# Kernel tuning notes

Measured on AMD Instinct MI355X. Metric: run time of the kernel, lower is better.

## Reference

```python
import jax, jax.numpy as jnp
import numpy as np

N_EMBD = 2048
N_HEAD = 16
HEAD_DIM = N_EMBD // N_HEAD
BATCH = 2
SEQ = 2048


def setup_inputs() -> dict:
    key = jax.random.key(0)
    k1, k2, k3 = jax.random.split(key, 3)
    scale = 0.02
    return {
        "hidden_states": jax.random.normal(k1, (BATCH, SEQ, N_EMBD), dtype=jnp.float32),
        "c_attn_w": jax.random.normal(k2, (N_EMBD, 3 * N_EMBD), dtype=jnp.float32) * scale,
        "c_attn_b": jnp.zeros((3 * N_EMBD,), dtype=jnp.float32),
        "c_proj_w": jax.random.normal(k3, (N_EMBD, N_EMBD), dtype=jnp.float32) * scale,
        "c_proj_b": jnp.zeros((N_EMBD,), dtype=jnp.float32),
    }


def reference(hidden_states, c_attn_w, c_attn_b, c_proj_w, c_proj_b):
    B, S, E = hidden_states.shape
    # Fused QKV projection (Conv1D: x @ W + b)
    qkv = hidden_states @ c_attn_w + c_attn_b  # [B, S, 3E]
    q, k, v = jnp.split(qkv, 3, axis=-1)
    # split heads -> [B, H, S, D]
    def split_heads(t):
        return t.reshape(B, S, N_HEAD, HEAD_DIM).transpose(0, 2, 1, 3)
    q, k, v = split_heads(q), split_heads(k), split_heads(v)
    # scaled scores, causal mask, softmax (dropout p=0 -> identity)
    scores = jnp.einsum("bhqd,bhkd->bhqk", q, k) / jnp.asarray(
        HEAD_DIM ** 0.5, dtype=q.dtype)
    causal = jnp.tril(jnp.ones((S, S), dtype=bool))  # [S, S]
    mask_value = jnp.finfo(scores.dtype).min
    scores = jnp.where(causal[None, None, :, :], scores, mask_value)
    attn = jax.nn.softmax(scores, axis=-1)
    out = jnp.einsum("bhqk,bhkd->bhqd", attn, v)  # [B, H, S, D]
    # merge heads -> [B, S, E]
    out = out.transpose(0, 2, 1, 3).reshape(B, S, E)
    # output projection
    return out @ c_proj_w + c_proj_b
```

## Files before the change

### kernel.cpp

```cpp
#include <hip/hip_runtime.h>
#include <hip/hip_bf16.h>

typedef __bf16 bf16x8 __attribute__((ext_vector_type(8)));
typedef float f32x4 __attribute__((ext_vector_type(4)));

__device__ __forceinline__ float bf2f(unsigned short u) {
  union { unsigned int i; float f; } v; v.i = ((unsigned int)u) << 16; return v.f;
}
__device__ __forceinline__ unsigned short f2bf(float f) {
  union { unsigned int i; float f; } v; v.f = f;
  unsigned int i = v.i;
  return (unsigned short)((i + 0x7FFFu + ((i >> 16) & 1u)) >> 16);
}

typedef const __attribute__((address_space(1))) unsigned int* gas_ptr;
typedef __attribute__((address_space(3))) unsigned int* las_ptr;
__device__ __forceinline__ void gload_lds16(const unsigned short* g, unsigned short* l) {
  __builtin_amdgcn_global_load_lds((gas_ptr)(const void*)g, (las_ptr)(void*)l, 16, 0, 0);
}

__global__ __launch_bounds__(256) void prologue_k(const void* __restrict__ hidden,
                                                  const void* __restrict__ w_qkv,
                                                  const void* __restrict__ w_proj,
                                                  unsigned short* __restrict__ hidden_bf,
                                                  unsigned short* __restrict__ Wt_qkv,
                                                  unsigned short* __restrict__ Wt_proj,
                                                  int* __restrict__ flag) {
  __shared__ unsigned short tile[32][33];
  __shared__ int s4[4];
  const int t = threadIdx.x;
  {
    const unsigned short* h = (const unsigned short*)hidden;
    int cnt = 0;
    for (int i = t; i < 2048; i += 256) {
      unsigned short u = h[2 * i];
      int e = (u >> 7) & 0xFF;
      cnt += ((e >= 96 && e <= 140) || u == 0) ? 1 : 0;
    }
#pragma unroll
    for (int off = 1; off < 64; off <<= 1) cnt += __shfl_xor(cnt, off, 64);
    if ((t & 63) == 0) s4[t >> 6] = cnt;
  }
  __syncthreads();
  const int f = (s4[0] + s4[1] + s4[2] + s4[3]) >= 1800;
  if (blockIdx.x == 0 && t == 0) *flag = f;

  int bid = blockIdx.x;
  if (bid < 2048) {
    if (f) return;
    const float* src = (const float*)hidden;
    int base = bid * 4096;
#pragma unroll
    for (int k = 0; k < 16; k++) hidden_bf[base + t + 256 * k] = f2bf(src[base + t + 256 * k]);
    return;
  }
  const void* src; unsigned short* dst; int C, cx, cy;
  if (bid < 14336) { bid -= 2048;  src = w_qkv;  dst = Wt_qkv;  C = 6144; cx = bid % 192; cy = bid / 192; }
  else             { bid -= 14336; src = w_proj; dst = Wt_proj; C = 2048; cx = bid % 64;  cy = bid / 64;  }
  const int x = t & 31, y = t >> 5;
  const int r0 = cy * 32, c0 = cx * 32;
#pragma unroll
  for (int i = 0; i < 4; i++) {
    size_t idx = (size_t)(r0 + y + 8 * i) * C + c0 + x;
    tile[y + 8 * i][x] = f ? ((const unsigned short*)src)[idx]
                           : f2bf(((const float*)src)[idx]);
  }
  __syncthreads();
#pragma unroll
  for (int i = 0; i < 4; i++)
    dst[(size_t)(c0 + y + 8 * i) * 2048 + r0 + x] = tile[x][y + 8 * i];
}

__global__ __launch_bounds__(256) void gemm_bias_k(const unsigned short* __restrict__ A_bf,
                                                   const unsigned short* __restrict__ A_cvt,
                                                   const unsigned short* __restrict__ Bt,
                                                   const void* __restrict__ bias,
                                                   void* __restrict__ Cout,
                                                   unsigned short* __restrict__ Vt,
                                                   int M, int N, int K,
                                                   const int* __restrict__ flag,
                                                   int final_out, int v_fuse) {
  __shared__ __attribute__((aligned(16))) unsigned short smem[2][128][64];
#define As smem[0]
#define Bs smem[1]
  const int f = *flag;
  const unsigned short* A = f ? A_bf : A_cvt;
  const int t = threadIdx.x;
  const int wave = t >> 6, lane = t & 63;
  const int col = lane & 15, quad = lane >> 4;
  const int wm = wave >> 1, wn = wave & 1;
  const int m0 = blockIdx.y * 128, n0 = blockIdx.x * 128;
  const int srow = lane >> 3;
  const int schunk = ((lane & 7) ^ srow) * 8;
  const int rsw = col & 7;

  const f32x4 fzero = {0.f, 0.f, 0.f, 0.f};
  f32x4 acc[4][4];
#pragma unroll
  for (int i = 0; i < 4; i++)
#pragma unroll
    for (int j = 0; j < 4; j++) acc[i][j] = fzero;

  for (int k0 = 0; k0 < K; k0 += 64) {
    __syncthreads();
#pragma unroll
    for (int c = 0; c < 4; c++) {
      int seg = wave * 4 + c;
      int row = seg * 8 + srow;
      gload_lds16(&A [(size_t)(m0 + row) * K + k0 + schunk], &As[seg * 8][0]);
      gload_lds16(&Bt[(size_t)(n0 + row) * K + k0 + schunk], &Bs[seg * 8][0]);
    }
    __syncthreads();
#pragma unroll
    for (int ks = 0; ks < 2; ks++) {
      bf16x8 af[4], bfr[4];
#pragma unroll
      for (int i = 0; i < 4; i++)
        af[i] = *(const bf16x8*)&As[wm * 64 + i * 16 + col][(((ks << 2) | quad) ^ rsw) * 8];
#pragma unroll
      for (int j = 0; j < 4; j++)
        bfr[j] = *(const bf16x8*)&Bs[wn * 64 + j * 16 + col][(((ks << 2) | quad) ^ rsw) * 8];
#pragma unroll
      for (int i = 0; i < 4; i++)
#pragma unroll
        for (int j = 0; j < 4; j++)
          acc[i][j] = __builtin_amdgcn_mfma_f32_16x16x32_bf16(af[i], bfr[j], acc[i][j], 0, 0, 0);
    }
  }

  if (v_fuse && n0 >= 4096) {
    const int bb = m0 >> 11, hh = (n0 - 4096) >> 7, s0k = m0 & 2047;
    unsigned short* Tr = &smem[0][0][0];
#pragma unroll
    for (int half = 0; half < 2; half++) {
      __syncthreads();
      if (wn == half) {
#pragma unroll
        for (int j = 0; j < 4; j++) {
          int n = n0 + wn * 64 + j * 16 + col;
          float bv = f ? bf2f(((const unsigned short*)bias)[n]) : ((const float*)bias)[n];
          int dloc = j * 16 + col;
#pragma unroll
          for (int i = 0; i < 4; i++)
#pragma unroll
            for (int r = 0; r < 4; r++)
              Tr[dloc * 130 + wm * 64 + i * 16 + quad * 4 + r] = f2bf(acc[i][j][r] + bv);
        }
      }
      __syncthreads();
      const int r2 = t >> 2, seg = (t & 3) * 32;
      size_t gaddr = (((size_t)(bb * 16 + hh)) * 128 + half * 64 + r2) * 2048 + s0k + seg;
#pragma unroll
      for (int c = 0; c < 4; c++)
        *(bf16x8*)&Vt[gaddr + c * 8] = *(const bf16x8*)&Tr[r2 * 130 + seg + c * 8];
    }
    return;
  }

  const int f32o = final_out ? (f == 0) : 0;
#pragma unroll
  for (int j = 0; j < 4; j++) {
    int n = n0 + wn * 64 + j * 16 + col;
    float bv = f ? bf2f(((const unsigned short*)bias)[n]) : ((const float*)bias)[n];
#pragma unroll
    for (int i = 0; i < 4; i++)
#pragma unroll
      for (int r = 0; r < 4; r++) {
        int m = m0 + wm * 64 + i * 16 + quad * 4 + r;
        float v = acc[i][j][r] + bv;
        if (f32o) ((float*)Cout)[(size_t)m * N + n] = v;
        else      ((unsigned short*)Cout)[(size_t)m * N + n] = f2bf(v);
      }
  }
#undef As
#undef Bs
}

#define ATT_SCALE_L2E 0.12751743f
__global__ __launch_bounds__(256) void attn_k(const unsigned short* __restrict__ qkv,
                                              const unsigned short* __restrict__ Vt,
                                              unsigned short* __restrict__ O) {
  __shared__ __attribute__((aligned(16))) unsigned short Ks[64][136];
  __shared__ __attribute__((aligned(16))) unsigned short Vs[128][72];
  __shared__ __attribute__((aligned(16))) unsigned short Ps[4][16][72];
  const int t = threadIdx.x;
  const int wave = t >> 6, lane = t & 63;
  const int col = lane & 15, quad = lane >> 4;
  const int h = blockIdx.y, b = blockIdx.z;
  const size_t base = (size_t)b * 2048 * 6144;
  const size_t vbase = ((size_t)(b * 16 + h)) * 128 * 2048;
  const int hcol = h * 128;

  const int kr = t >> 2;
  const int kc = (t & 3) * 8;
  const int vr = t >> 1;
  const int vc = (t & 1) * 32;

  const f32x4 fzero = {0.f, 0.f, 0.f, 0.f};

  for (int pass = 0; pass < 2; pass++) {
    const int qt = pass ? (int)blockIdx.x : 31 - (int)blockIdx.x;

    bf16x8 qf[4];
    {
      size_t qrow = base + (size_t)(qt * 64 + wave * 16 + col) * 6144 + hcol;
#pragma unroll
      for (int ks = 0; ks < 4; ks++)
        qf[ks] = *(const bf16x8*)&qkv[qrow + ks * 32 + quad * 8];
    }

    f32x4 o[8];
#pragma unroll
    for (int i = 0; i < 8; i++) o[i] = fzero;
    float l_i[4] = {0.f, 0.f, 0.f, 0.f};

    __syncthreads();
    {
      size_t grow = base + (size_t)kr * 6144 + 2048 + hcol;
#pragma unroll
      for (int p = 0; p < 4; p++)
        *(bf16x8*)&Ks[kr][kc + p * 32] = *(const bf16x8*)&qkv[grow + kc + p * 32];
      size_t vrow = vbase + (size_t)vr * 2048;
#pragma unroll
      for (int c = 0; c < 4; c++)
        *(bf16x8*)&Vs[vr][vc + c * 8] = *(const bf16x8*)&Vt[vrow + vc + c * 8];
    }
    __syncthreads();

    for (int kt = 0; kt <= qt; kt++) {
      bf16x8 kreg[4], vreg[4];
      const bool pf = (kt < qt);
      if (pf) {
        size_t grow = base + (size_t)((kt + 1) * 64 + kr) * 6144 + 2048 + hcol;
#pragma unroll
        for (int p = 0; p < 4; p++)
          kreg[p] = *(const bf16x8*)&qkv[grow + kc + p * 32];
        size_t vrow = vbase + (size_t)vr * 2048 + (kt + 1) * 64;
#pragma unroll
        for (int c = 0; c < 4; c++)
          vreg[c] = *(const bf16x8*)&Vt[vrow + vc + c * 8];
      }

      f32x4 sc[4];
#pragma unroll
      for (int nb = 0; nb < 4; nb++) {
        f32x4 s = fzero;
#pragma unroll
        for (int ks = 0; ks < 4; ks++) {
          bf16x8 kf = *(const bf16x8*)&Ks[nb * 16 + col][ks * 32 + quad * 8];
          s = __builtin_amdgcn_mfma_f32_16x16x32_bf16(qf[ks], kf, s, 0, 0, 0);
        }
        sc[nb] = s;
      }

      const bool diag = (kt == qt);
#pragma unroll
      for (int nb = 0; nb < 4; nb++) {
        int kl = nb * 16 + col;
#pragma unroll
        for (int r = 0; r < 4; r++) {
          float s = sc[nb][r];
          if (diag && kl > wave * 16 + quad * 4 + r) s = -1e30f;
          float p = exp2f(s * ATT_SCALE_L2E);
          l_i[r] += p;
          Ps[wave][quad * 4 + r][nb * 16 + col] = f2bf(p);
        }
      }
      bf16x8 pfr[2];
#pragma unroll
      for (int ks2 = 0; ks2 < 2; ks2++)
        pfr[ks2] = *(const bf16x8*)&Ps[wave][col][ks2 * 32 + quad * 8];
#pragma unroll
      for (int nbo = 0; nbo < 8; nbo++)
#pragma unroll
        for (int ks2 = 0; ks2 < 2; ks2++) {
          bf16x8 vf = *(const bf16x8*)&Vs[nbo * 16 + col][ks2 * 32 + quad * 8];
          o[nbo] = __builtin_amdgcn_mfma_f32_16x16x32_bf16(pfr[ks2], vf, o[nbo], 0, 0, 0);
        }

      __syncthreads();
      if (pf) {
#pragma unroll
        for (int p = 0; p < 4; p++)
          *(bf16x8*)&Ks[kr][kc + p * 32] = kreg[p];
#pragma unroll
        for (int c = 0; c < 4; c++)
          *(bf16x8*)&Vs[vr][vc + c * 8] = vreg[c];
      }
      __syncthreads();
    }

#pragma unroll
    for (int r = 0; r < 4; r++) {
#pragma unroll
      for (int off = 1; off < 16; off <<= 1)
        l_i[r] += __shfl_xor(l_i[r], off, 64);
      l_i[r] = 1.0f / l_i[r];
    }

#pragma unroll
    for (int nbo = 0; nbo < 8; nbo++)
#pragma unroll
      for (int r = 0; r < 4; r++) {
        int m = qt * 64 + wave * 16 + quad * 4 + r;
        O[((size_t)b * 2048 + m) * 2048 + hcol + nbo * 16 + col] = f2bf(o[nbo][r] * l_i[r]);
      }
  }
}

extern "C" void kernel_launch(void* const* d_in, const int* in_sizes, int n_in,
                              void* d_out, int out_size, void* d_ws, size_t ws_size,
                              hipStream_t stream) {
  (void)in_sizes; (void)n_in; (void)out_size; (void)ws_size;
  int* flag = (int*)d_ws;
  unsigned short* wsu = (unsigned short*)d_ws + 128;
  unsigned short* Wt_qkv    = wsu;
  unsigned short* Wt_proj   = Wt_qkv + (size_t)6144 * 2048;
  unsigned short* QKV       = Wt_proj + (size_t)2048 * 2048;
  unsigned short* hidden_bf = QKV + (size_t)4096 * 6144;
  unsigned short* Vt        = hidden_bf + (size_t)4096 * 2048;
  unsigned short* Obuf      = Wt_qkv;

  prologue_k<<<18432, 256, 0, stream>>>(d_in[0], d_in[1], d_in[3],
                                        hidden_bf, Wt_qkv, Wt_proj, flag);
  gemm_bias_k<<<dim3(48, 32), 256, 0, stream>>>((const unsigned short*)d_in[0], hidden_bf,
                                                Wt_qkv, d_in[2], QKV, Vt,
                                                4096, 6144, 2048, flag, 0, 1);
  attn_k<<<dim3(16, 16, 2), 256, 0, stream>>>(QKV, Vt, Obuf);
  gemm_bias_k<<<dim3(16, 32), 256, 0, stream>>>(Obuf, Obuf, Wt_proj, d_in[4], d_out, Vt,
                                                4096, 2048, 2048, flag, 1, 0);
}
```

Measured before the change: 439.5 us.

## Double-buffer attention K/V tiles with direct global-to-LDS loads, separate V transpose

The attention kernel now stages K and V tiles through two LDS buffers, filled by global_load_lds with an XOR-swizzled layout. This replaces the register prefetch and its extra barrier-guarded store step, so the next tile loads while the current one computes. The V transpose that was fused into the QKV GEMM epilogue moves to a separate small transpose kernel, which simplifies the GEMM but adds a launch and an extra pass over V. Workspace buffers are reassigned so Vt reuses the QKV-weight region and the attention output reuses the hidden_bf region.

```diff
diff --git a/kernel.cpp b/kernel.cpp
--- a/kernel.cpp
+++ b/kernel.cpp
@@ -71,18 +71,33 @@
     dst[(size_t)(c0 + y + 8 * i) * 2048 + r0 + x] = tile[x][y + 8 * i];
 }
 
+__global__ __launch_bounds__(256) void transpose_v_k(const unsigned short* __restrict__ qkv,
+                                                     unsigned short* __restrict__ Vt) {
+  __shared__ unsigned short tile[32][33];
+  const int bh = blockIdx.z;
+  const int b = bh >> 4, hh = bh & 15;
+  const int s0 = blockIdx.x * 32, d0 = blockIdx.y * 32;
+  const int x = threadIdx.x & 31, y = threadIdx.x >> 5;
+#pragma unroll
+  for (int i = 0; i < 4; i++)
+    tile[y + 8 * i][x] =
+        qkv[((size_t)b * 2048 + s0 + y + 8 * i) * 6144 + 4096 + hh * 128 + d0 + x];
+  __syncthreads();
+#pragma unroll
+  for (int i = 0; i < 4; i++)
+    Vt[((size_t)bh * 128 + d0 + y + 8 * i) * 2048 + s0 + x] = tile[x][y + 8 * i];
+}
+
 __global__ __launch_bounds__(256) void gemm_bias_k(const unsigned short* __restrict__ A_bf,
                                                    const unsigned short* __restrict__ A_cvt,
                                                    const unsigned short* __restrict__ Bt,
                                                    const void* __restrict__ bias,
                                                    void* __restrict__ Cout,
-                                                   unsigned short* __restrict__ Vt,
                                                    int M, int N, int K,
                                                    const int* __restrict__ flag,
-                                                   int final_out, int v_fuse) {
-  __shared__ __attribute__((aligned(16))) unsigned short smem[2][128][64];
-#define As smem[0]
-#define Bs smem[1]
+                                                   int final_out) {
+  __shared__ __attribute__((aligned(16))) unsigned short As[128][64];
+  __shared__ __attribute__((aligned(16))) unsigned short Bs[128][64];
   const int f = *flag;
   const unsigned short* A = f ? A_bf : A_cvt;
   const int t = threadIdx.x;
@@ -127,36 +142,6 @@
           acc[i][j] = __builtin_amdgcn_mfma_f32_16x16x32_bf16(af[i], bfr[j], acc[i][j], 0, 0, 0);
     }
   }
-
-  if (v_fuse && n0 >= 4096) {
-    const int bb = m0 >> 11, hh = (n0 - 4096) >> 7, s0k = m0 & 2047;
-    unsigned short* Tr = &smem[0][0][0];
-#pragma unroll
-    for (int half = 0; half < 2; half++) {
-      __syncthreads();
-      if (wn == half) {
-#pragma unroll
-        for (int j = 0; j < 4; j++) {
-          int n = n0 + wn * 64 + j * 16 + col;
-          float bv = f ? bf2f(((const unsigned short*)bias)[n]) : ((const float*)bias)[n];
-          int dloc = j * 16 + col;
-#pragma unroll
-          for (int i = 0; i < 4; i++)
-#pragma unroll
-            for (int r = 0; r < 4; r++)
-              Tr[dloc * 130 + wm * 64 + i * 16 + quad * 4 + r] = f2bf(acc[i][j][r] + bv);
-        }
-      }
-      __syncthreads();
-      const int r2 = t >> 2, seg = (t & 3) * 32;
-      size_t gaddr = (((size_t)(bb * 16 + hh)) * 128 + half * 64 + r2) * 2048 + s0k + seg;
-#pragma unroll
-      for (int c = 0; c < 4; c++)
-        *(bf16x8*)&Vt[gaddr + c * 8] = *(const bf16x8*)&Tr[r2 * 130 + seg + c * 8];
-    }
-    return;
-  }
-
   const int f32o = final_out ? (f == 0) : 0;
 #pragma unroll
   for (int j = 0; j < 4; j++) {
@@ -172,16 +157,14 @@
         else      ((unsigned short*)Cout)[(size_t)m * N + n] = f2bf(v);
       }
   }
-#undef As
-#undef Bs
 }
 
 #define ATT_SCALE_L2E 0.12751743f
 __global__ __launch_bounds__(256) void attn_k(const unsigned short* __restrict__ qkv,
                                               const unsigned short* __restrict__ Vt,
                                               unsigned short* __restrict__ O) {
-  __shared__ __attribute__((aligned(16))) unsigned short Ks[64][136];
-  __shared__ __attribute__((aligned(16))) unsigned short Vs[128][72];
+  __shared__ __attribute__((aligned(16))) unsigned short Ks[2][64][128];
+  __shared__ __attribute__((aligned(16))) unsigned short Vs[2][128][64];
   __shared__ __attribute__((aligned(16))) unsigned short Ps[4][16][72];
   const int t = threadIdx.x;
   const int wave = t >> 6, lane = t & 63;
@@ -191,10 +174,11 @@
   const size_t vbase = ((size_t)(b * 16 + h)) * 128 * 2048;
   const int hcol = h * 128;
 
-  const int kr = t >> 2;
-  const int kc = (t & 3) * 8;
-  const int vr = t >> 1;
-  const int vc = (t & 1) * 32;
+  const int k_rl = lane >> 4;
+  const int k_ch = lane & 15;
+  const int v_dl = lane >> 3;
+  const int v_ch = ((lane & 7) ^ (v_dl & 7)) * 8;
+  const int rsw = col & 7;
 
   const f32x4 fzero = {0.f, 0.f, 0.f, 0.f};
 
@@ -215,30 +199,31 @@
     float l_i[4] = {0.f, 0.f, 0.f, 0.f};
 
     __syncthreads();
-    {
-      size_t grow = base + (size_t)kr * 6144 + 2048 + hcol;
-#pragma unroll
-      for (int p = 0; p < 4; p++)
-        *(bf16x8*)&Ks[kr][kc + p * 32] = *(const bf16x8*)&qkv[grow + kc + p * 32];
-      size_t vrow = vbase + (size_t)vr * 2048;
-#pragma unroll
-      for (int c = 0; c < 4; c++)
-        *(bf16x8*)&Vs[vr][vc + c * 8] = *(const bf16x8*)&Vt[vrow + vc + c * 8];
+#pragma unroll
+    for (int c = 0; c < 4; c++) {
+      int i = wave * 4 + c;
+      int row = 4 * i + k_rl;
+      int sch = (k_ch ^ (row & 7)) * 8;
+      gload_lds16(&qkv[base + (size_t)row * 6144 + 2048 + hcol + sch], &Ks[0][4 * i][0]);
+      int d = 8 * i + v_dl;
+      gload_lds16(&Vt[vbase + (size_t)d * 2048 + v_ch], &Vs[0][8 * i][0]);
     }
     __syncthreads();
 
     for (int kt = 0; kt <= qt; kt++) {
-      bf16x8 kreg[4], vreg[4];
-      const bool pf = (kt < qt);
-      if (pf) {
-        size_t grow = base + (size_t)((kt + 1) * 64 + kr) * 6144 + 2048 + hcol;
-#pragma unroll
-        for (int p = 0; p < 4; p++)
-          kreg[p] = *(const bf16x8*)&qkv[grow + kc + p * 32];
-        size_t vrow = vbase + (size_t)vr * 2048 + (kt + 1) * 64;
-#pragma unroll
-        for (int c = 0; c < 4; c++)
-          vreg[c] = *(const bf16x8*)&Vt[vrow + vc + c * 8];
+      const int buf = kt & 1;
+      if (kt < qt) {
+        const int nb1 = buf ^ 1;
+#pragma unroll
+        for (int c = 0; c < 4; c++) {
+          int i = wave * 4 + c;
+          int row = 4 * i + k_rl;
+          int sch = (k_ch ^ (row & 7)) * 8;
+          gload_lds16(&qkv[base + (size_t)((kt + 1) * 64 + row) * 6144 + 2048 + hcol + sch],
+                      &Ks[nb1][4 * i][0]);
+          int d = 8 * i + v_dl;
+          gload_lds16(&Vt[vbase + (size_t)d * 2048 + (kt + 1) * 64 + v_ch], &Vs[nb1][8 * i][0]);
+        }
       }
 
       f32x4 sc[4];
@@ -247,7 +232,7 @@
         f32x4 s = fzero;
 #pragma unroll
         for (int ks = 0; ks < 4; ks++) {
-          bf16x8 kf = *(const bf16x8*)&Ks[nb * 16 + col][ks * 32 + quad * 8];
+          bf16x8 kf = *(const bf16x8*)&Ks[buf][nb * 16 + col][(((ks << 2) | quad) ^ rsw) * 8];
           s = __builtin_amdgcn_mfma_f32_16x16x32_bf16(qf[ks], kf, s, 0, 0, 0);
         }
         sc[nb] = s;
@@ -271,22 +256,15 @@
       for (int ks2 = 0; ks2 < 2; ks2++)
         pfr[ks2] = *(const bf16x8*)&Ps[wave][col][ks2 * 32 + quad * 8];
 #pragma unroll
-      for (int nbo = 0; nbo < 8; nbo++)
+      for (int nbo = 0; nbo < 8; nbo++) {
+        const int d = nbo * 16 + col;
 #pragma unroll
         for (int ks2 = 0; ks2 < 2; ks2++) {
-          bf16x8 vf = *(const bf16x8*)&Vs[nbo * 16 + col][ks2 * 32 + quad * 8];
+          bf16x8 vf = *(const bf16x8*)&Vs[buf][d][(((ks2 << 2) | quad) ^ rsw) * 8];
           o[nbo] = __builtin_amdgcn_mfma_f32_16x16x32_bf16(pfr[ks2], vf, o[nbo], 0, 0, 0);
         }
-
-      __syncthreads();
-      if (pf) {
-#pragma unroll
-        for (int p = 0; p < 4; p++)
-          *(bf16x8*)&Ks[kr][kc + p * 32] = kreg[p];
-#pragma unroll
-        for (int c = 0; c < 4; c++)
-          *(bf16x8*)&Vs[vr][vc + c * 8] = vreg[c];
-      }
+      }
+
       __syncthreads();
     }
 
@@ -318,15 +296,16 @@
   unsigned short* Wt_proj   = Wt_qkv + (size_t)6144 * 2048;
   unsigned short* QKV       = Wt_proj + (size_t)2048 * 2048;
   unsigned short* hidden_bf = QKV + (size_t)4096 * 6144;
-  unsigned short* Vt        = hidden_bf + (size_t)4096 * 2048;
-  unsigned short* Obuf      = Wt_qkv;
+  unsigned short* Vt        = Wt_qkv;
+  unsigned short* Obuf      = hidden_bf;
 
   prologue_k<<<18432, 256, 0, stream>>>(d_in[0], d_in[1], d_in[3],
                                         hidden_bf, Wt_qkv, Wt_proj, flag);
   gemm_bias_k<<<dim3(48, 32), 256, 0, stream>>>((const unsigned short*)d_in[0], hidden_bf,
-                                                Wt_qkv, d_in[2], QKV, Vt,
-                                                4096, 6144, 2048, flag, 0, 1);
+                                                Wt_qkv, d_in[2], QKV,
+                                                4096, 6144, 2048, flag, 0);
+  transpose_v_k<<<dim3(64, 4, 32), 256, 0, stream>>>(QKV, Vt);
   attn_k<<<dim3(16, 16, 2), 256, 0, stream>>>(QKV, Vt, Obuf);
-  gemm_bias_k<<<dim3(16, 32), 256, 0, stream>>>(Obuf, Obuf, Wt_proj, d_in[4], d_out, Vt,
-                                                4096, 2048, 2048, flag, 1, 0);
-}
+  gemm_bias_k<<<dim3(16, 32), 256, 0, stream>>>(Obuf, Obuf, Wt_proj, d_in[4], d_out,
+                                                4096, 2048, 2048, flag, 1);
+}
```

Result: faster. 429.5 us (-2.3%).
